# Performance work log

Measured on AMD Instinct MI355X. Metric: run time of the kernel, lower is better.

The kernel has to match this reference:

```python
import jax, jax.numpy as jnp
import numpy as np
from itertools import combinations

DIM = 3
METRIC = np.array([1.0, 1.0, 1.0], dtype=np.float32)
KERNEL_SIZE = 7
C_IN, C_OUT = 32, 32
HIDDEN = 64
NUM_LAYERS = 4
N_GRID = KERNEL_SIZE ** DIM


def _build_cayley(dim, metric):
    blades = [()] + [c for r in range(1, dim + 1) for c in combinations(range(dim), r)]
    idx = {b: i for i, b in enumerate(blades)}
    n = len(blades)
    C = np.zeros((n, n, n), dtype=np.float32)
    for i, a in enumerate(blades):
        for j, b in enumerate(blades):
            arr = list(a) + list(b)
            sign = 1.0
            changed = True
            while changed:
                changed = False
                t = 0
                while t < len(arr) - 1:
                    if arr[t] == arr[t + 1]:
                        sign *= metric[arr[t]]
                        del arr[t:t + 2]
                        changed = True
                        break
                    if arr[t] > arr[t + 1]:
                        arr[t], arr[t + 1] = arr[t + 1], arr[t]
                        sign = -sign
                        changed = True
                    t += 1
            C[i, j, idx[tuple(arr)]] = sign
    grades = np.array([len(b) for b in blades])
    return C, grades

_C_LRO, GRADES = _build_cayley(DIM, METRIC)
CAYLEY = np.transpose(_C_LRO, (0, 2, 1))  # [left, out, right] (CEGNN convention)
N_BLADES = CAYLEY.shape[0]
N_GRADES = DIM + 1

# nonzero grade-triple paths of the Cayley tensor and blade-level path-id lookup
_gp = np.zeros((N_GRADES,) * 3, dtype=bool)
for a in range(N_GRADES):
    for b in range(N_GRADES):
        for c in range(N_GRADES):
            _gp[a, b, c] = np.any(CAYLEY[np.ix_(GRADES == a, GRADES == b, GRADES == c)] != 0)
PATHS = np.argwhere(_gp)
P = len(PATHS)
assert P == 20  # product_paths_sum for Cl(3,0)
_pid = -np.ones((N_GRADES,) * 3, dtype=np.int64)
for p, (a, b, c) in enumerate(PATHS):
    _pid[a, b, c] = p
BLADE_PID = _pid[GRADES[:, None, None], GRADES[None, :, None], GRADES[None, None, :]]
BLADE_PID = np.where(BLADE_PID < 0, P, BLADE_PID)  # P -> zero slot

# centered relative-position grid, (N, 1, dim)
_ax = np.arange(KERNEL_SIZE, dtype=np.float32) - (KERNEL_SIZE - 1) / 2.0
_grid = np.stack(np.meshgrid(*([_ax] * DIM), indexing='ij'), axis=-1).reshape(-1, DIM)
REL_POS = jnp.asarray(_grid[:, None, :])
CAYLEY_J = jnp.asarray(CAYLEY)
GRADE_ONEHOT = jnp.asarray((GRADES[:, None] == np.arange(N_GRADES)[None, :]).astype(np.float32))
FACTOR = 1.0 / np.sqrt(float(KERNEL_SIZE ** DIM))
BLADES_OF = {g: np.where(GRADES == g)[0] for g in range(N_GRADES)}


def embed_grade(x, g):
    out = jnp.zeros(x.shape[:-1] + (N_BLADES,), x.dtype)
    return out.at[..., BLADES_OF[g]].set(x)


def expand_paths(w):
    # (..., P) grade-path weights -> (..., B, B, B) blade-level weights
    wz = jnp.concatenate([w, jnp.zeros(w.shape[:-1] + (1,), w.dtype)], axis=-1)
    return wz[..., BLADE_PID]


def mv_linear(x, W, b):
    # grade-wise equivariant channel mixing; x: (N,Ci,B), W: (G,Co,Ci), bias on scalar blade
    y = jnp.einsum('boi,nib->nob', W[GRADES], x)
    return y.at[:, :, 0].add(b)


def mv_silu(x, a, b):
    # gate each grade by sigmoid of its (learned-scaled) squared norm
    qg = jnp.einsum('ncb,bg->ncg', x * x, GRADE_ONEHOT)
    gate = jax.nn.sigmoid(a * qg + b)
    return x * gate[:, :, GRADES]


def gp_layer(x, w):
    # fully-connected steerable geometric product; x: (N,C,B), w: (Co,C,P)
    wc = expand_paths(w) * CAYLEY_J  # (Co, C, B, B, B)
    y = jnp.einsum('nik,oikjm,nim->noj', x, wc, x)
    return y / np.sqrt(float(x.shape[1]))


def setup_inputs() -> dict:
    key = jax.random.key(0)
    ks = jax.random.split(key, 8)
    G, B, H, Pn = N_GRADES, N_BLADES, HIDDEN, P
    rn = lambda k, s, sc: jax.random.normal(k, s, dtype=jnp.float32) * sc
    ci1 = C_IN + 1
    return {
        'condition': rn(ks[0], (C_IN, B), 1.0),
        'rel_pos_sigma': jnp.ones((1, 1, 1), jnp.float32),
        'cayley_w': rn(ks[1], (C_OUT, C_IN, Pn), 1.0 / np.sqrt(C_IN)),
        'lin0_W': rn(ks[2], (G, H, ci1), 1.0 / np.sqrt(ci1)),
        'lin0_b': jnp.zeros((H,), jnp.float32),
        'act0_a': rn(ks[3], (H, G), 0.2),
        'act0_b': jnp.zeros((H, G), jnp.float32),
        'gps_w': rn(ks[4], (NUM_LAYERS, H, H, Pn), 0.5 / np.sqrt(H)),
        'lins_W': rn(ks[5], (NUM_LAYERS - 1, G, H, H), 1.0 / np.sqrt(H)),
        'lins_b': jnp.zeros((NUM_LAYERS - 1, H), jnp.float32),
        'acts_a': rn(ks[6], (NUM_LAYERS - 1, H, G), 0.2),
        'acts_b': jnp.zeros((NUM_LAYERS - 1, H, G), jnp.float32),
        'out_W': rn(ks[7], (G, C_OUT * C_IN, H), 1.0 / np.sqrt(H)),
        'out_b': jnp.zeros((C_OUT * C_IN,), jnp.float32),
        'shell_sigma': jnp.ones((1, C_OUT, C_IN, B), jnp.float32),
    }


def reference(condition, rel_pos_sigma, cayley_w, lin0_W, lin0_b, act0_a, act0_b,
              gps_w, lins_W, lins_b, acts_a, acts_b, out_W, out_b, shell_sigma):
    metric = jnp.asarray(METRIC)
    q = jnp.sum(metric * REL_POS * REL_POS, axis=-1, keepdims=True)  # (N,1,1)
    scalar = jnp.exp(-q / (2.0 * rel_pos_sigma ** 2))
    x = embed_grade(scalar, 0) + embed_grade(REL_POS, 1)  # (N,1,B)
    cond = jnp.broadcast_to(condition[None], (N_GRID,) + condition.shape)
    x = jnp.concatenate([x, cond], axis=1)  # (N, c_in+1, B)
    # kernel network: CEGNN blocks [MVLinear -> MVSiLU -> steerable geometric product]
    h = gp_layer(mv_silu(mv_linear(x, lin0_W, lin0_b), act0_a, act0_b), gps_w[0])
    for l in range(NUM_LAYERS - 1):
        h = gp_layer(mv_silu(mv_linear(h, lins_W[l], lins_b[l]), acts_a[l], acts_b[l]), gps_w[l + 1])
    k = mv_linear(h, out_W, out_b).reshape(N_GRID, C_OUT, C_IN, N_BLADES)
    # per-(c_out,c_in,blade) scalar radial shell
    shell = jnp.exp(-q.reshape(N_GRID, 1, 1, 1) / (shell_sigma ** 2))
    k = k * shell * FACTOR
    # kernel head: sparse weighted-Cayley contraction
    wc = expand_paths(cayley_w) * CAYLEY_J  # (c_out, c_in, B, B, B)
    K = jnp.einsum('noik,oiklm->olimn', k, wc)
    return K.reshape(C_OUT * N_BLADES, C_IN * N_BLADES, KERNEL_SIZE, KERNEL_SIZE, KERNEL_SIZE)
```

## Files before the change

### kernel.cpp

```cpp
#include <hip/hip_runtime.h>
#include <math.h>

#define NGRID 343
#define NPATH 20

struct Tab {
  int prod_idx[8][8];
  int prod_sgn[8][8];
  int pid[4][4][4];
  int grade[8];
  int kk_idx[8][8];
  int kk_sgn[8][8];
};

constexpr Tab make_tab() {
  Tab t{};
  int mask[8]  = {0,1,2,4,3,5,6,7};
  int idxof[8] = {0,1,2,4,3,5,6,7};
  for (int k = 0; k < 8; ++k) {
    int g = 0;
    for (int b = 0; b < 3; ++b) g += (mask[k] >> b) & 1;
    t.grade[k] = g;
  }
  for (int k = 0; k < 8; ++k)
    for (int m = 0; m < 8; ++m) {
      int A = mask[k], B = mask[m];
      t.prod_idx[k][m] = idxof[A ^ B];
      int c = 0;
      for (int i = 0; i < 3; ++i)
        if ((B >> i) & 1)
          for (int j = i + 1; j < 3; ++j)
            if ((A >> j) & 1) c++;
      t.prod_sgn[k][m] = (c & 1) ? -1 : 1;
    }
  int pc = 0;
  for (int a = 0; a < 4; ++a)
    for (int b = 0; b < 4; ++b)
      for (int c = 0; c < 4; ++c) {
        bool ok = false;
        for (int k = 0; k < 8; ++k)
          for (int m = 0; m < 8; ++m)
            if (t.grade[k] == a && t.grade[m] == c &&
                t.grade[t.prod_idx[k][m]] == b)
              ok = true;
        t.pid[a][b][c] = ok ? pc++ : NPATH;
      }
  for (int l = 0; l < 8; ++l)
    for (int m = 0; m < 8; ++m)
      for (int k = 0; k < 8; ++k)
        if (t.prod_idx[k][m] == l) {
          t.kk_idx[l][m] = k;
          t.kk_sgn[l][m] = t.prod_sgn[k][m];
        }
  return t;
}
constexpr Tab TB = make_tab();

__device__ __forceinline__ int gradeOf(int b) {
  return (b == 0) ? 0 : (b < 4) ? 1 : (b < 7) ? 2 : 3;
}

#define OFF_LIN0T 0
#define OFF_GPST  8448
#define OFF_OUTWT 336128
#define OFF_KWS   598272

__global__ void ccs_prep_kernel(const float* __restrict__ lin0_W,
                                const float* __restrict__ gps_w,
                                const float* __restrict__ out_W,
                                float* __restrict__ ws) {
  const int TOT = 8448 + 327680 + 262144;
  for (int d = blockIdx.x * blockDim.x + threadIdx.x; d < TOT;
       d += gridDim.x * blockDim.x) {
    float v;
    if (d < 8448) {
      int hh = d & 63, ch = (d >> 6) % 33, g = (d >> 6) / 33;
      v = lin0_W[(g * 64 + hh) * 33 + ch];
    } else if (d < OFF_OUTWT) {
      int idx = d - OFF_GPST;
      int p = idx % 20, r = idx / 20;
      int o = r & 63, i = (r >> 6) & 63, l = r >> 12;
      v = gps_w[(((size_t)l * 64 + o) * 64 + i) * 20 + p];
    } else {
      int idx = d - OFF_OUTWT;
      int g = idx & 3, i = (idx >> 2) & 63, oc = idx >> 8;
      v = out_W[(g * 1024 + oc) * 64 + i];
    }
    ws[d] = v;
  }
}

__global__ __launch_bounds__(1024, 4)
void ccs_net_kernel(const float* __restrict__ condition,
                    const float* __restrict__ rel_pos_sigma,
                    const float* __restrict__ lin0_b,
                    const float* __restrict__ act0_a,
                    const float* __restrict__ act0_b,
                    const float* __restrict__ lins_W,
                    const float* __restrict__ lins_b,
                    const float* __restrict__ acts_a,
                    const float* __restrict__ acts_b,
                    const float* __restrict__ out_b,
                    const float* __restrict__ shell_sigma,
                    const float* __restrict__ ws,
                    float* __restrict__ kws) {
  const float* lin0t = ws + OFF_LIN0T;
  const float* gpst  = ws + OFF_GPST;
  const float* outwt = ws + OFF_OUTWT;

  __shared__ __align__(16) float xb[264];
  __shared__ __align__(16) float F0[512];
  __shared__ __align__(16) float F1[512];
  __shared__ __align__(16) float part[8192];

  const int n = blockIdx.x;
  const int tid = threadIdx.x;
  const int iz = n % 7, iy = (n / 7) % 7, ix = n / 49;
  const float px = (float)ix - 3.f, py = (float)iy - 3.f, pz = (float)iz - 3.f;
  const float q = px * px + py * py + pz * pz;
  const float sig = rel_pos_sigma[0];
  const float scal = expf(-q / (2.f * sig * sig));

  if (tid < 264) {
    int ch = tid >> 3, b = tid & 7;
    float v;
    if (ch == 0)
      v = (b == 0) ? scal : (b == 1) ? px : (b == 2) ? py : (b == 3) ? pz : 0.f;
    else
      v = condition[(ch - 1) * 8 + b];
    xb[tid] = v;
  }
  __syncthreads();

  const int hh = tid & 63;
  const int bb = (tid >> 6) & 7;
  const bool act512 = tid < 512;

  if (act512) {
    int g = gradeOf(bb);
    float acc = (bb == 0) ? lin0_b[hh] : 0.f;
    const float* wrow = lin0t + g * (33 * 64) + hh;
    #pragma unroll
    for (int ch = 0; ch < 33; ++ch)
      acc = fmaf(wrow[ch * 64], xb[ch * 8 + bb], acc);
    F0[bb * 64 + hh] = acc;
  }
  __syncthreads();

  auto silu = [&](const float* src, float* dst, const float* aa,
                  const float* ab) {
    if (act512) {
      int g = gradeOf(bb);
      int s0 = (g == 0) ? 0 : (g == 1) ? 1 : (g == 2) ? 4 : 7;
      int cnt = (g == 0 || g == 3) ? 1 : 3;
      float qg = 0.f;
      for (int u = 0; u < cnt; ++u) {
        float v = src[(s0 + u) * 64 + hh];
        qg = fmaf(v, v, qg);
      }
      float z = fmaf(aa[hh * 4 + g], qg, ab[hh * 4 + g]);
      float gate = 1.f / (1.f + expf(-z));
      dst[bb * 64 + hh] = src[bb * 64 + hh] * gate;
    }
  };

  auto lin = [&](const float* src, float* dst, const float* wl,
                 const float* bias) {
    if (act512) {
      int g = gradeOf(bb);
      float acc = (bb == 0) ? bias[hh] : 0.f;
      const float4* wr = (const float4*)(wl + ((size_t)g * 64 + hh) * 64);
      #pragma unroll
      for (int u = 0; u < 16; ++u) {
        float4 w = wr[u];
        const float* s = src + bb * 64 + u * 4;
        acc = fmaf(w.x, s[0], acc);
        acc = fmaf(w.y, s[1], acc);
        acc = fmaf(w.z, s[2], acc);
        acc = fmaf(w.w, s[3], acc);
      }
      dst[bb * 64 + hh] = acc;
    }
  };

  auto gp = [&](const float* src, float* dst, const float* wl, bool imaj) {
    const int o = tid & 63;
    const int isub = tid >> 6;
    float facc[8];
    #pragma unroll
    for (int j = 0; j < 8; ++j) facc[j] = 0.f;
    #pragma unroll
    for (int it = 0; it < 4; ++it) {
      const int i = isub * 4 + it;
      float x8[8];
      #pragma unroll
      for (int b = 0; b < 8; ++b) x8[b] = src[b * 64 + i];
      float4 w4[5];
      const float4* wb = (const float4*)(wl + ((size_t)i * 64 + o) * 20);
      #pragma unroll
      for (int u = 0; u < 5; ++u) w4[u] = wb[u];
      const float* wp = (const float*)w4;
      #pragma unroll
      for (int k = 0; k < 8; ++k) {
        const int p = TB.pid[TB.grade[k]][0][TB.grade[k]];
        float tp = x8[k] * x8[k];
        facc[0] = fmaf(TB.prod_sgn[k][k] > 0 ? tp : -tp, wp[p], facc[0]);
      }
      #pragma unroll
      for (int k = 0; k < 8; ++k) {
        #pragma unroll
        for (int m = k + 1; m < 8; ++m) {
          const int j  = TB.prod_idx[k][m];
          const int p1 = TB.pid[TB.grade[k]][TB.grade[j]][TB.grade[m]];
          const int p2 = TB.pid[TB.grade[m]][TB.grade[j]][TB.grade[k]];
          const float w1 = (TB.prod_sgn[k][m] > 0) ? wp[p1] : -wp[p1];
          const float w2 = (TB.prod_sgn[m][k] > 0) ? wp[p2] : -wp[p2];
          facc[j] = fmaf(x8[k] * x8[m], w1 + w2, facc[j]);
        }
      }
    }
    #pragma unroll
    for (int j = 0; j < 8; ++j) part[(j * 16 + isub) * 64 + o] = facc[j];
    __syncthreads();
    if (act512) {
      const int o2 = tid & 63, j2 = tid >> 6;
      float s = 0.f;
      #pragma unroll
      for (int u = 0; u < 16; ++u) s += part[(j2 * 16 + u) * 64 + o2];
      s *= 0.125f;
      if (imaj)
        dst[o2 * 8 + j2] = s;
      else
        dst[j2 * 64 + o2] = s;
    }
    __syncthreads();
  };

  silu(F0, F1, act0_a, act0_b);
  __syncthreads();
  gp(F1, F0, gpst + 0, false);

  float* f = F0;
  float* g_ = F1;
  #pragma unroll 1
  for (int l = 0; l < 3; ++l) {
    lin(f, g_, lins_W + (size_t)l * 16384, lins_b + l * 64);
    __syncthreads();
    silu(g_, f, acts_a + l * 256, acts_b + l * 256);
    __syncthreads();
    gp(f, g_, gpst + (size_t)(l + 1) * 81920, l == 2);
    float* t = f; f = g_; g_ = t;
  }

  const float FACTOR = 1.0f / sqrtf(343.0f);
  const int oc = tid;
  float acc[8];
  #pragma unroll
  for (int b = 0; b < 8; ++b) acc[b] = 0.f;
  acc[0] = out_b[oc];
  const float4* wv = (const float4*)(outwt + (size_t)oc * 256);
  #pragma unroll 8
  for (int i = 0; i < 64; ++i) {
    float4 w = wv[i];
    const float4* hp = (const float4*)(f + i * 8);
    float4 h0 = hp[0], h1 = hp[1];
    acc[0] = fmaf(w.x, h0.x, acc[0]);
    acc[1] = fmaf(w.y, h0.y, acc[1]);
    acc[2] = fmaf(w.y, h0.z, acc[2]);
    acc[3] = fmaf(w.y, h0.w, acc[3]);
    acc[4] = fmaf(w.z, h1.x, acc[4]);
    acc[5] = fmaf(w.z, h1.y, acc[5]);
    acc[6] = fmaf(w.z, h1.z, acc[6]);
    acc[7] = fmaf(w.w, h1.w, acc[7]);
  }
  float4 s0 = ((const float4*)(shell_sigma + oc * 8))[0];
  float4 s1 = ((const float4*)(shell_sigma + oc * 8))[1];
  float o8[8];
  o8[0] = acc[0] * expf(-q / (s0.x * s0.x)) * FACTOR;
  o8[1] = acc[1] * expf(-q / (s0.y * s0.y)) * FACTOR;
  o8[2] = acc[2] * expf(-q / (s0.z * s0.z)) * FACTOR;
  o8[3] = acc[3] * expf(-q / (s0.w * s0.w)) * FACTOR;
  o8[4] = acc[4] * expf(-q / (s1.x * s1.x)) * FACTOR;
  o8[5] = acc[5] * expf(-q / (s1.y * s1.y)) * FACTOR;
  o8[6] = acc[6] * expf(-q / (s1.z * s1.z)) * FACTOR;
  o8[7] = acc[7] * expf(-q / (s1.w * s1.w)) * FACTOR;
  float4* dst = (float4*)(kws + ((size_t)n * 1024 + oc) * 8);
  dst[0] = make_float4(o8[0], o8[1], o8[2], o8[3]);
  dst[1] = make_float4(o8[4], o8[5], o8[6], o8[7]);
}

__global__ __launch_bounds__(256)
void ccs_expand_kernel(const float* __restrict__ cayley_w,
                       const float* __restrict__ kws,
                       float* __restrict__ out) {
  const int oi = blockIdx.x;
  const int o = oi >> 5, i = oi & 31;
  const int tid = threadIdx.x;
  __shared__ float sk[343 * 9];

  for (int idx = tid; idx < 686; idx += 256) {
    int nn = idx >> 1, h = (idx & 1) * 4;
    float4 v = *(const float4*)(kws + ((size_t)nn * 1024 + oi) * 8 + h);
    float* s = sk + nn * 9 + h;
    s[0] = v.x; s[1] = v.y; s[2] = v.z; s[3] = v.w;
  }
  float cw[20];
  #pragma unroll
  for (int p = 0; p < 20; ++p) cw[p] = cayley_w[oi * 20 + p];
  __syncthreads();

  #pragma unroll
  for (int l = 0; l < 8; ++l) {
    #pragma unroll
    for (int m = 0; m < 8; ++m) {
      const int kk = TB.kk_idx[l][m];
      const int p = TB.pid[TB.grade[kk]][TB.grade[l]][TB.grade[m]];
      const float wv = (TB.kk_sgn[l][m] > 0) ? cw[p] : -cw[p];
      float* orow = out + ((size_t)((o * 8 + l) * 256 + i * 8 + m)) * 343;
      for (int c = tid; c < 343; c += 256) orow[c] = sk[c * 9 + kk] * wv;
    }
  }
}

extern "C" void kernel_launch(void* const* d_in, const int* in_sizes, int n_in,
                              void* d_out, int out_size, void* d_ws,
                              size_t ws_size, hipStream_t stream) {
  const float* condition     = (const float*)d_in[0];
  const float* rel_pos_sigma = (const float*)d_in[1];
  const float* cayley_w      = (const float*)d_in[2];
  const float* lin0_W        = (const float*)d_in[3];
  const float* lin0_b        = (const float*)d_in[4];
  const float* act0_a        = (const float*)d_in[5];
  const float* act0_b        = (const float*)d_in[6];
  const float* gps_w         = (const float*)d_in[7];
  const float* lins_W        = (const float*)d_in[8];
  const float* lins_b        = (const float*)d_in[9];
  const float* acts_a        = (const float*)d_in[10];
  const float* acts_b        = (const float*)d_in[11];
  const float* out_W         = (const float*)d_in[12];
  const float* out_b         = (const float*)d_in[13];
  const float* shell_sigma   = (const float*)d_in[14];

  float* ws = (float*)d_ws;
  float* kws = ws + OFF_KWS;
  float* out = (float*)d_out;

  ccs_prep_kernel<<<dim3(640), dim3(256), 0, stream>>>(lin0_W, gps_w, out_W,
                                                       ws);
  ccs_net_kernel<<<dim3(343), dim3(1024), 0, stream>>>(
      condition, rel_pos_sigma, lin0_b, act0_a, act0_b, lins_W, lins_b, acts_a,
      acts_b, out_b, shell_sigma, ws, kws);
  ccs_expand_kernel<<<dim3(1024), dim3(256), 0, stream>>>(cayley_w, kws, out);
}
```

Baseline: 262.7 us.

## Split output projection into batched kernel and shrink net blocks to 256 threads

The per-grid-point network kernel now runs 256 threads per block and does more work per thread, so each geometric-product weight read covers 16 input channels and the reduction scratch shrinks. The final output projection moves into a separate kernel that processes 8 grid points per block with a transposed weight layout. This lets each output weight load be reused across several points instead of being re-read by all 343 blocks. The expand kernel is split over two grid dimensions to add parallelism. In exchange there is an extra kernel launch and a hidden-state round trip through global memory.

```diff
diff --git a/kernel.cpp b/kernel.cpp
--- a/kernel.cpp
+++ b/kernel.cpp
@@ -64,6 +64,7 @@
 #define OFF_GPST  8448
 #define OFF_OUTWT 336128
 #define OFF_KWS   598272
+#define OFF_HBUF  3408128
 
 __global__ void ccs_prep_kernel(const float* __restrict__ lin0_W,
                                 const float* __restrict__ gps_w,
@@ -83,14 +84,14 @@
       v = gps_w[(((size_t)l * 64 + o) * 64 + i) * 20 + p];
     } else {
       int idx = d - OFF_OUTWT;
-      int g = idx & 3, i = (idx >> 2) & 63, oc = idx >> 8;
+      int oc = idx & 1023, g = (idx >> 10) & 3, i = idx >> 12;
       v = out_W[(g * 1024 + oc) * 64 + i];
     }
     ws[d] = v;
   }
 }
 
-__global__ __launch_bounds__(1024, 4)
+__global__ __launch_bounds__(256)
 void ccs_net_kernel(const float* __restrict__ condition,
                     const float* __restrict__ rel_pos_sigma,
                     const float* __restrict__ lin0_b,
@@ -100,18 +101,15 @@
                     const float* __restrict__ lins_b,
                     const float* __restrict__ acts_a,
                     const float* __restrict__ acts_b,
-                    const float* __restrict__ out_b,
-                    const float* __restrict__ shell_sigma,
                     const float* __restrict__ ws,
-                    float* __restrict__ kws) {
+                    float* __restrict__ hbuf) {
   const float* lin0t = ws + OFF_LIN0T;
   const float* gpst  = ws + OFF_GPST;
-  const float* outwt = ws + OFF_OUTWT;
 
   __shared__ __align__(16) float xb[264];
   __shared__ __align__(16) float F0[512];
   __shared__ __align__(16) float F1[512];
-  __shared__ __align__(16) float part[8192];
+  __shared__ __align__(16) float part[2048];
 
   const int n = blockIdx.x;
   const int tid = threadIdx.x;
@@ -121,36 +119,39 @@
   const float sig = rel_pos_sigma[0];
   const float scal = expf(-q / (2.f * sig * sig));
 
-  if (tid < 264) {
-    int ch = tid >> 3, b = tid & 7;
+  for (int t = tid; t < 264; t += 256) {
+    int ch = t >> 3, b = t & 7;
     float v;
     if (ch == 0)
       v = (b == 0) ? scal : (b == 1) ? px : (b == 2) ? py : (b == 3) ? pz : 0.f;
     else
       v = condition[(ch - 1) * 8 + b];
-    xb[tid] = v;
+    xb[t] = v;
   }
   __syncthreads();
 
   const int hh = tid & 63;
-  const int bb = (tid >> 6) & 7;
-  const bool act512 = tid < 512;
-
-  if (act512) {
-    int g = gradeOf(bb);
-    float acc = (bb == 0) ? lin0_b[hh] : 0.f;
+  const int brow = tid >> 6;
+
+  #pragma unroll
+  for (int rep = 0; rep < 2; ++rep) {
+    int b = brow + 4 * rep;
+    int g = gradeOf(b);
+    float acc = (b == 0) ? lin0_b[hh] : 0.f;
     const float* wrow = lin0t + g * (33 * 64) + hh;
     #pragma unroll
     for (int ch = 0; ch < 33; ++ch)
-      acc = fmaf(wrow[ch * 64], xb[ch * 8 + bb], acc);
-    F0[bb * 64 + hh] = acc;
+      acc = fmaf(wrow[ch * 64], xb[ch * 8 + b], acc);
+    F0[b * 64 + hh] = acc;
   }
   __syncthreads();
 
   auto silu = [&](const float* src, float* dst, const float* aa,
                   const float* ab) {
-    if (act512) {
-      int g = gradeOf(bb);
+    #pragma unroll
+    for (int rep = 0; rep < 2; ++rep) {
+      int b = brow + 4 * rep;
+      int g = gradeOf(b);
       int s0 = (g == 0) ? 0 : (g == 1) ? 1 : (g == 2) ? 4 : 7;
       int cnt = (g == 0 || g == 3) ? 1 : 3;
       float qg = 0.f;
@@ -160,26 +161,28 @@
       }
       float z = fmaf(aa[hh * 4 + g], qg, ab[hh * 4 + g]);
       float gate = 1.f / (1.f + expf(-z));
-      dst[bb * 64 + hh] = src[bb * 64 + hh] * gate;
+      dst[b * 64 + hh] = src[b * 64 + hh] * gate;
     }
   };
 
   auto lin = [&](const float* src, float* dst, const float* wl,
                  const float* bias) {
-    if (act512) {
-      int g = gradeOf(bb);
-      float acc = (bb == 0) ? bias[hh] : 0.f;
+    #pragma unroll
+    for (int rep = 0; rep < 2; ++rep) {
+      int b = brow + 4 * rep;
+      int g = gradeOf(b);
+      float acc = (b == 0) ? bias[hh] : 0.f;
       const float4* wr = (const float4*)(wl + ((size_t)g * 64 + hh) * 64);
       #pragma unroll
       for (int u = 0; u < 16; ++u) {
         float4 w = wr[u];
-        const float* s = src + bb * 64 + u * 4;
-        acc = fmaf(w.x, s[0], acc);
-        acc = fmaf(w.y, s[1], acc);
-        acc = fmaf(w.z, s[2], acc);
-        acc = fmaf(w.w, s[3], acc);
+        float4 s = *(const float4*)(src + b * 64 + u * 4);
+        acc = fmaf(w.x, s.x, acc);
+        acc = fmaf(w.y, s.y, acc);
+        acc = fmaf(w.z, s.z, acc);
+        acc = fmaf(w.w, s.w, acc);
       }
-      dst[bb * 64 + hh] = acc;
+      dst[b * 64 + hh] = acc;
     }
   };
 
@@ -189,16 +192,16 @@
     float facc[8];
     #pragma unroll
     for (int j = 0; j < 8; ++j) facc[j] = 0.f;
-    #pragma unroll
-    for (int it = 0; it < 4; ++it) {
-      const int i = isub * 4 + it;
+    const float4* wb = (const float4*)(wl + (size_t)((isub * 16) * 64 + o) * 20);
+    #pragma unroll 4
+    for (int it = 0; it < 16; ++it) {
+      const int i = isub * 16 + it;
+      float4 w4[5];
+      #pragma unroll
+      for (int u = 0; u < 5; ++u) w4[u] = wb[it * 320 + u];
       float x8[8];
       #pragma unroll
       for (int b = 0; b < 8; ++b) x8[b] = src[b * 64 + i];
-      float4 w4[5];
-      const float4* wb = (const float4*)(wl + ((size_t)i * 64 + o) * 20);
-      #pragma unroll
-      for (int u = 0; u < 5; ++u) w4[u] = wb[u];
       const float* wp = (const float*)w4;
       #pragma unroll
       for (int k = 0; k < 8; ++k) {
@@ -220,13 +223,14 @@
       }
     }
     #pragma unroll
-    for (int j = 0; j < 8; ++j) part[(j * 16 + isub) * 64 + o] = facc[j];
+    for (int j = 0; j < 8; ++j) part[(j * 4 + isub) * 64 + o] = facc[j];
     __syncthreads();
-    if (act512) {
-      const int o2 = tid & 63, j2 = tid >> 6;
-      float s = 0.f;
-      #pragma unroll
-      for (int u = 0; u < 16; ++u) s += part[(j2 * 16 + u) * 64 + o2];
+    #pragma unroll
+    for (int rep = 0; rep < 2; ++rep) {
+      int idx = tid + rep * 256;
+      int j2 = idx >> 6, o2 = idx & 63;
+      float s = part[(j2 * 4 + 0) * 64 + o2] + part[(j2 * 4 + 1) * 64 + o2] +
+                part[(j2 * 4 + 2) * 64 + o2] + part[(j2 * 4 + 3) * 64 + o2];
       s *= 0.125f;
       if (imaj)
         dst[o2 * 8 + j2] = s;
@@ -252,41 +256,80 @@
     float* t = f; f = g_; g_ = t;
   }
 
+  if (tid < 128)
+    ((float4*)(hbuf + (size_t)n * 512))[tid] = ((const float4*)f)[tid];
+}
+
+__global__ __launch_bounds__(256)
+void ccs_out_kernel(const float* __restrict__ out_b,
+                    const float* __restrict__ shell_sigma,
+                    const float* __restrict__ ws,
+                    const float* __restrict__ hbuf,
+                    float* __restrict__ kws) {
+  const float* outwt = ws + OFF_OUTWT;
+  const int tid = threadIdx.x;
+  const int oc = blockIdx.x * 256 + tid;
+  const int n0 = blockIdx.y * 8;
+  const int nn = (n0 + 8 <= NGRID) ? 8 : (NGRID - n0);
+
+  __shared__ __align__(16) float sh[8 * 512];
+  for (int idx = tid; idx < nn * 128; idx += 256)
+    ((float4*)sh)[idx] = ((const float4*)(hbuf + (size_t)n0 * 512))[idx];
+  __syncthreads();
+
+  float acc[8][8];
+  const float bias = out_b[oc];
+  #pragma unroll
+  for (int np = 0; np < 8; ++np) {
+    #pragma unroll
+    for (int b = 0; b < 8; ++b) acc[np][b] = 0.f;
+    acc[np][0] = bias;
+  }
+
+  #pragma unroll 4
+  for (int i = 0; i < 64; ++i) {
+    const float w0 = outwt[(i * 4 + 0) * 1024 + oc];
+    const float w1 = outwt[(i * 4 + 1) * 1024 + oc];
+    const float w2 = outwt[(i * 4 + 2) * 1024 + oc];
+    const float w3 = outwt[(i * 4 + 3) * 1024 + oc];
+    #pragma unroll
+    for (int np = 0; np < 8; ++np) {
+      const float* h = sh + np * 512 + i * 8;
+      float4 h0 = ((const float4*)h)[0];
+      float4 h1 = ((const float4*)h)[1];
+      acc[np][0] = fmaf(w0, h0.x, acc[np][0]);
+      acc[np][1] = fmaf(w1, h0.y, acc[np][1]);
+      acc[np][2] = fmaf(w1, h0.z, acc[np][2]);
+      acc[np][3] = fmaf(w1, h0.w, acc[np][3]);
+      acc[np][4] = fmaf(w2, h1.x, acc[np][4]);
+      acc[np][5] = fmaf(w2, h1.y, acc[np][5]);
+      acc[np][6] = fmaf(w2, h1.z, acc[np][6]);
+      acc[np][7] = fmaf(w3, h1.w, acc[np][7]);
+    }
+  }
+
   const float FACTOR = 1.0f / sqrtf(343.0f);
-  const int oc = tid;
-  float acc[8];
-  #pragma unroll
-  for (int b = 0; b < 8; ++b) acc[b] = 0.f;
-  acc[0] = out_b[oc];
-  const float4* wv = (const float4*)(outwt + (size_t)oc * 256);
-  #pragma unroll 8
-  for (int i = 0; i < 64; ++i) {
-    float4 w = wv[i];
-    const float4* hp = (const float4*)(f + i * 8);
-    float4 h0 = hp[0], h1 = hp[1];
-    acc[0] = fmaf(w.x, h0.x, acc[0]);
-    acc[1] = fmaf(w.y, h0.y, acc[1]);
-    acc[2] = fmaf(w.y, h0.z, acc[2]);
-    acc[3] = fmaf(w.y, h0.w, acc[3]);
-    acc[4] = fmaf(w.z, h1.x, acc[4]);
-    acc[5] = fmaf(w.z, h1.y, acc[5]);
-    acc[6] = fmaf(w.z, h1.z, acc[6]);
-    acc[7] = fmaf(w.w, h1.w, acc[7]);
-  }
   float4 s0 = ((const float4*)(shell_sigma + oc * 8))[0];
   float4 s1 = ((const float4*)(shell_sigma + oc * 8))[1];
-  float o8[8];
-  o8[0] = acc[0] * expf(-q / (s0.x * s0.x)) * FACTOR;
-  o8[1] = acc[1] * expf(-q / (s0.y * s0.y)) * FACTOR;
-  o8[2] = acc[2] * expf(-q / (s0.z * s0.z)) * FACTOR;
-  o8[3] = acc[3] * expf(-q / (s0.w * s0.w)) * FACTOR;
-  o8[4] = acc[4] * expf(-q / (s1.x * s1.x)) * FACTOR;
-  o8[5] = acc[5] * expf(-q / (s1.y * s1.y)) * FACTOR;
-  o8[6] = acc[6] * expf(-q / (s1.z * s1.z)) * FACTOR;
-  o8[7] = acc[7] * expf(-q / (s1.w * s1.w)) * FACTOR;
-  float4* dst = (float4*)(kws + ((size_t)n * 1024 + oc) * 8);
-  dst[0] = make_float4(o8[0], o8[1], o8[2], o8[3]);
-  dst[1] = make_float4(o8[4], o8[5], o8[6], o8[7]);
+  for (int np = 0; np < nn; ++np) {
+    const int n = n0 + np;
+    const int iz = n % 7, iy = (n / 7) % 7, ix = n / 49;
+    const float px = (float)ix - 3.f, py = (float)iy - 3.f,
+                pz = (float)iz - 3.f;
+    const float q = px * px + py * py + pz * pz;
+    float o8[8];
+    o8[0] = acc[np][0] * expf(-q / (s0.x * s0.x)) * FACTOR;
+    o8[1] = acc[np][1] * expf(-q / (s0.y * s0.y)) * FACTOR;
+    o8[2] = acc[np][2] * expf(-q / (s0.z * s0.z)) * FACTOR;
+    o8[3] = acc[np][3] * expf(-q / (s0.w * s0.w)) * FACTOR;
+    o8[4] = acc[np][4] * expf(-q / (s1.x * s1.x)) * FACTOR;
+    o8[5] = acc[np][5] * expf(-q / (s1.y * s1.y)) * FACTOR;
+    o8[6] = acc[np][6] * expf(-q / (s1.z * s1.z)) * FACTOR;
+    o8[7] = acc[np][7] * expf(-q / (s1.w * s1.w)) * FACTOR;
+    float4* dst = (float4*)(kws + ((size_t)n * 1024 + oc) * 8);
+    dst[0] = make_float4(o8[0], o8[1], o8[2], o8[3]);
+    dst[1] = make_float4(o8[4], o8[5], o8[6], o8[7]);
+  }
 }
 
 __global__ __launch_bounds__(256)
@@ -295,6 +338,7 @@
                        float* __restrict__ out) {
   const int oi = blockIdx.x;
   const int o = oi >> 5, i = oi & 31;
+  const int l0 = blockIdx.y * 4;
   const int tid = threadIdx.x;
   __shared__ float sk[343 * 9];
 
@@ -310,7 +354,8 @@
   __syncthreads();
 
   #pragma unroll
-  for (int l = 0; l < 8; ++l) {
+  for (int dl = 0; dl < 4; ++dl) {
+    const int l = l0 + dl;
     #pragma unroll
     for (int m = 0; m < 8; ++m) {
       const int kk = TB.kk_idx[l][m];
@@ -343,12 +388,16 @@
 
   float* ws = (float*)d_ws;
   float* kws = ws + OFF_KWS;
+  float* hbuf = ws + OFF_HBUF;
   float* out = (float*)d_out;
 
   ccs_prep_kernel<<<dim3(640), dim3(256), 0, stream>>>(lin0_W, gps_w, out_W,
                                                        ws);
-  ccs_net_kernel<<<dim3(343), dim3(1024), 0, stream>>>(
+  ccs_net_kernel<<<dim3(343), dim3(256), 0, stream>>>(
       condition, rel_pos_sigma, lin0_b, act0_a, act0_b, lins_W, lins_b, acts_a,
-      acts_b, out_b, shell_sigma, ws, kws);
-  ccs_expand_kernel<<<dim3(1024), dim3(256), 0, stream>>>(cayley_w, kws, out);
-}
+      acts_b, ws, hbuf);
+  ccs_out_kernel<<<dim3(4, 43), dim3(256), 0, stream>>>(out_b, shell_sigma, ws,
+                                                        hbuf, kws);
+  ccs_expand_kernel<<<dim3(1024, 2), dim3(256), 0, stream>>>(cayley_w, kws,
+                                                             out);
+}
```

After: 283.4 us. 1.08x slower.
